# Kernel optimization log

Measured on AMD Instinct MI355X. Metric: run time of the kernel, lower is better.

## Reference

```python
import jax, jax.numpy as jnp
import numpy as np

B, T, D = 2, 2048, 1024
H, HD = 16, 64           # num_heads, head_dim (key_dim = value_dim = H*HD = D)
K = 4                    # short conv kernel size
EPS = 1e-6


def setup_inputs() -> dict:
    key = jax.random.key(0)
    ks = jax.random.split(key, 16)
    w = lambda k, shape, s=0.02: jax.random.normal(k, shape, jnp.float32) * s
    dt = jnp.exp(jax.random.uniform(ks[12], (H,)) * (np.log(0.1) - np.log(0.001)) + np.log(0.001))
    dt = jnp.clip(dt, 0.0001, None)
    return {
        "hidden_states": jax.random.normal(ks[0], (B, T, D), jnp.float32),
        "Wq": w(ks[1], (H * HD, D)),
        "Wk": w(ks[2], (H * HD, D)),
        "Wv": w(ks[3], (H * HD, D)),
        "Wa": w(ks[4], (H, D)),
        "Wb": w(ks[5], (H, D)),
        "Wg": w(ks[6], (H * HD, D)),
        "Wo": w(ks[7], (D, H * HD)),
        "q_norm_w": jnp.ones((HD,), jnp.float32),
        "k_norm_w": jnp.ones((HD,), jnp.float32),
        "o_norm_w": jnp.ones((HD,), jnp.float32),
        "A_log": jnp.log(jax.random.uniform(ks[11], (H,), jnp.float32, 0.5, 8.0)),
        "dt_bias": dt + jnp.log(-jnp.expm1(-dt)),
        "conv_q_w": w(ks[13], (H * HD, K), 0.2),
        "conv_k_w": w(ks[14], (H * HD, K), 0.2),
        "conv_v_w": w(ks[15], (H * HD, K), 0.2),
    }


def _short_conv_silu(x, w):
    # causal depthwise conv1d (kernel K) + SiLU; x: [B,T,C], w: [C,K]
    xc = jnp.transpose(x, (0, 2, 1))                       # [B,C,T]
    y = jax.lax.conv_general_dilated(
        xc, w[:, None, :], (1,), [(w.shape[-1] - 1, 0)],
        dimension_numbers=("NCH", "OIH", "NCH"), feature_group_count=w.shape[0])
    y = jnp.transpose(y, (0, 2, 1))
    return y * jax.nn.sigmoid(y)


def _rmsnorm(x, w):
    return x * jax.lax.rsqrt(jnp.mean(x * x, -1, keepdims=True) + EPS) * w


def _l2norm(x):
    return x * jax.lax.rsqrt(jnp.sum(x * x, -1, keepdims=True) + EPS)


def _forward(hidden_states, Wq, Wk, Wv, Wa, Wb, Wg, Wo,
             q_norm_w, k_norm_w, o_norm_w, A_log, dt_bias,
             conv_q_w, conv_k_w, conv_v_w):
    h = hidden_states
    q = _short_conv_silu(h @ Wq.T, conv_q_w).reshape(B, T, H, HD)
    k = _short_conv_silu(h @ Wk.T, conv_k_w).reshape(B, T, H, HD)
    v = _short_conv_silu(h @ Wv.T, conv_v_w).reshape(B, T, H, HD)
    q = _l2norm(_rmsnorm(q, q_norm_w))
    k = _l2norm(_rmsnorm(k, k_norm_w))
    beta = jax.nn.sigmoid(h @ Wb.T)                                  # [B,T,H]
    g = -jnp.exp(A_log) * jax.nn.softplus(h @ Wa.T + dt_bias)        # [B,T,H]
    scale = HD ** -0.5

    def step(S, inp):  # S: [B,H,dk,dv]
        qt, kt, vt, gt, bt = inp
        S = S * jnp.exp(gt)[:, :, None, None]
        kv = jnp.einsum("bhk,bhkv->bhv", kt, S)
        delta = (vt - kv) * bt[..., None]
        S = S + jnp.einsum("bhk,bhv->bhkv", kt, delta)
        o = jnp.einsum("bhk,bhkv->bhv", qt * scale, S)
        return S, o

    tm = lambda x: jnp.swapaxes(x, 0, 1)  # [B,T,...] -> [T,B,...]
    S0 = jnp.zeros((B, H, HD, HD), jnp.float32)
    _, o = jax.lax.scan(step, S0, (tm(q), tm(k), tm(v), tm(g), tm(beta)))
    o = jnp.swapaxes(o, 0, 1)                                        # [B,T,H,HD]

    gv = (h @ Wg.T).reshape(B, T, H, HD)
    o = _rmsnorm(o, o_norm_w) * (gv * jax.nn.sigmoid(gv))            # swish gate
    return o.reshape(B, T, H * HD) @ Wo.T


def reference(hidden_states, Wq, Wk, Wv, Wa, Wb, Wg, Wo,
              q_norm_w, k_norm_w, o_norm_w, A_log, dt_bias,
              conv_q_w, conv_k_w, conv_v_w):
    return _forward(hidden_states, Wq, Wk, Wv, Wa, Wb, Wg, Wo,
                    q_norm_w, k_norm_w, o_norm_w, A_log, dt_bias,
                    conv_q_w, conv_k_w, conv_v_w)
```

## Files before the change

kernel.cpp:

```cpp
#include <hip/hip_runtime.h>
#include <cstdint>
#include <cstddef>

#define B_ 2
#define T_ 2048
#define D_ 1024
#define H_ 16
#define HD_ 64
#define NC_ 32

typedef unsigned short u16;
typedef __attribute__((ext_vector_type(8))) short bf16x8;
typedef __attribute__((ext_vector_type(4))) float f32x4;

__device__ __forceinline__ float dot4(float4 a, float4 b, float acc) {
  return fmaf(a.x, b.x, fmaf(a.y, b.y, fmaf(a.z, b.z, fmaf(a.w, b.w, acc))));
}
__device__ __forceinline__ u16 f2bf(float f) {
  unsigned u = __float_as_uint(f);
  u += 0x7fffu + ((u >> 16) & 1u);
  return (u16)(u >> 16);
}
__device__ __forceinline__ float bf2f(u16 v) {
  return __uint_as_float(((unsigned)v) << 16);
}
__device__ __forceinline__ float4 ld4bf(const u16* p) {
  uint2 v = *(const uint2*)p;
  return float4{__uint_as_float(v.x << 16),
                __uint_as_float(v.x & 0xffff0000u),
                __uint_as_float(v.y << 16),
                __uint_as_float(v.y & 0xffff0000u)};
}
__device__ __forceinline__ bf16x8 pack8(float4 a, float4 b) {
  union { u16 us[8]; bf16x8 v; } p;
  p.us[0] = f2bf(a.x); p.us[1] = f2bf(a.y); p.us[2] = f2bf(a.z); p.us[3] = f2bf(a.w);
  p.us[4] = f2bf(b.x); p.us[5] = f2bf(b.y); p.us[6] = f2bf(b.z); p.us[7] = f2bf(b.w);
  return p.v;
}
__device__ __forceinline__ void glds16(const u16* g, u16* l) {
  __builtin_amdgcn_global_load_lds(
      (const __attribute__((address_space(1))) void*)g,
      (__attribute__((address_space(3))) void*)l, 16, 0, 0);
}
__device__ __forceinline__ float4 conv4(float4 x0, float4 x1, float4 x2, float4 x3,
                                        const float4* w) {
  float4 y;
  y.x = fmaf(w[0].x, x0.x, fmaf(w[0].y, x1.x, fmaf(w[0].z, x2.x, w[0].w * x3.x)));
  y.y = fmaf(w[1].x, x0.y, fmaf(w[1].y, x1.y, fmaf(w[1].z, x2.y, w[1].w * x3.y)));
  y.z = fmaf(w[2].x, x0.z, fmaf(w[2].y, x1.z, fmaf(w[2].z, x2.z, w[2].w * x3.z)));
  y.w = fmaf(w[3].x, x0.w, fmaf(w[3].y, x1.w, fmaf(w[3].z, x2.w, w[3].w * x3.w)));
  return y;
}
__device__ __forceinline__ float4 silu4(float4 a) {
  return float4{a.x / (1.f + __expf(-a.x)), a.y / (1.f + __expf(-a.y)),
                a.z / (1.f + __expf(-a.z)), a.w / (1.f + __expf(-a.w))};
}

__global__ __launch_bounds__(256) void cvt_all(
    const float* __restrict__ h, const float* __restrict__ w0,
    const float* __restrict__ w1, const float* __restrict__ w2,
    const float* __restrict__ w3, const float* __restrict__ w4,
    u16* __restrict__ h_bf, u16* __restrict__ wb)
{
  const int blk = blockIdx.x;
  const float* src;
  u16* dst;
  int lb;
  if (blk < 2048) { src = h; dst = h_bf; lb = blk; }
  else {
    int k = (blk - 2048) >> 9, r = (blk - 2048) & 511;
    src = k == 0 ? w0 : k == 1 ? w1 : k == 2 ? w2 : k == 3 ? w3 : w4;
    dst = wb + (size_t)k * 1048576;
    lb = r;
  }
  int i = (lb * 256 + threadIdx.x) * 8;
  float4 v0 = *(const float4*)(src + i);
  float4 v1 = *(const float4*)(src + i + 4);
  union { u16 us[8]; uint4 u4; } p;
  p.us[0] = f2bf(v0.x); p.us[1] = f2bf(v0.y); p.us[2] = f2bf(v0.z); p.us[3] = f2bf(v0.w);
  p.us[4] = f2bf(v1.x); p.us[5] = f2bf(v1.y); p.us[6] = f2bf(v1.z); p.us[7] = f2bf(v1.w);
  *(uint4*)(dst + i) = p.u4;
}

__device__ __forceinline__ void gemm_core256bf(const u16* __restrict__ A,
    const u16* __restrict__ Bw, u16* __restrict__ C,
    u16* As, u16* Bs, int row0, int col0, int K, int N)
{
  const int tid = threadIdx.x;
  const int lane = tid & 63, wave = tid >> 6;
  const int wr = (wave >> 1) * 128, wc = (wave & 1) * 64;
  const int lr = lane & 15, lkq = lane >> 4;
  const int lkp = (lkq ^ ((lr >> 1) & 3)) * 8;
  const int rql = (lane >> 2);
  const int cql = (((lane & 3) ^ ((rql >> 1) & 3))) * 8;
  const u16* gA[4];
  const u16* gB[2];
  #pragma unroll
  for (int i = 0; i < 4; ++i)
    gA[i] = A + (size_t)(row0 + (wave + 4*i) * 16 + rql) * K + cql;
  #pragma unroll
  for (int j = 0; j < 2; ++j)
    gB[j] = Bw + (size_t)(col0 + (wave + 4*j) * 16 + rql) * K + cql;

  f32x4 acc[8][4];
  #pragma unroll
  for (int i = 0; i < 8; ++i)
    #pragma unroll
    for (int j = 0; j < 4; ++j) acc[i][j] = f32x4{0.f, 0.f, 0.f, 0.f};

  auto STAGE = [&](int buf, int kt) {
    u16* ab = As + buf * 8192;
    u16* bb = Bs + buf * 4096;
    #pragma unroll
    for (int i = 0; i < 4; ++i) glds16(gA[i] + kt * 32, ab + (wave + 4*i) * 512);
    #pragma unroll
    for (int j = 0; j < 2; ++j) glds16(gB[j] + kt * 32, bb + (wave + 4*j) * 512);
  };

  const int KT = K >> 5;
  STAGE(0, 0);
  STAGE(1, 1);
  int cur = 0;
  for (int kt = 0; kt < KT; ++kt) {
    if (kt + 2 < KT) {
      STAGE(cur == 0 ? 2 : (cur == 1 ? 0 : 1), kt + 2);
      asm volatile("s_waitcnt vmcnt(12)" ::: "memory");
    } else if (kt + 1 < KT) {
      asm volatile("s_waitcnt vmcnt(6)" ::: "memory");
    } else {
      asm volatile("s_waitcnt vmcnt(0)" ::: "memory");
    }
    __builtin_amdgcn_s_barrier();
    __builtin_amdgcn_sched_barrier(0);
    const u16* Asc = As + cur * 8192;
    const u16* Bsc = Bs + cur * 4096;
    bf16x8 af[8], bf[4];
    #pragma unroll
    for (int i = 0; i < 8; ++i) af[i] = *(const bf16x8*)&Asc[(wr + i * 16 + lr) * 32 + lkp];
    #pragma unroll
    for (int j = 0; j < 4; ++j) bf[j] = *(const bf16x8*)&Bsc[(wc + j * 16 + lr) * 32 + lkp];
    #pragma unroll
    for (int i = 0; i < 8; ++i)
      #pragma unroll
      for (int j = 0; j < 4; ++j)
        acc[i][j] = __builtin_amdgcn_mfma_f32_16x16x32_bf16(af[i], bf[j], acc[i][j], 0, 0, 0);
    __builtin_amdgcn_sched_barrier(0);
    __builtin_amdgcn_s_barrier();
    cur = (cur == 2) ? 0 : cur + 1;
  }
  const int orow = row0 + wr + lkq * 4;
  const int ocol = col0 + wc + lr;
  #pragma unroll
  for (int i = 0; i < 8; ++i)
    #pragma unroll
    for (int j = 0; j < 4; ++j)
      #pragma unroll
      for (int r = 0; r < 4; ++r)
        C[(size_t)(orow + i * 16 + r) * N + ocol + j * 16] = f2bf(acc[i][j][r]);
}

__device__ __forceinline__ void gemm_core128(const u16* __restrict__ A,
    const u16* __restrict__ Bw, float* __restrict__ C,
    u16* As, u16* Bs, int row0, int col0, int K, int N)
{
  const int tid = threadIdx.x;
  const int lane = tid & 63, wave = tid >> 6;
  const int wr = (wave >> 1) * 64, wc = (wave & 1) * 64;
  const int lr = lane & 15;
  const int lkp = (((lane >> 4) ^ ((lr >> 1) & 3))) * 8;
  const int rql = (lane >> 2);
  const int cql = (((lane & 3) ^ ((rql >> 1) & 3))) * 8;
  const u16* gA0 = A + (size_t)(row0 + wave * 16 + rql) * K + cql;
  const u16* gA1 = A + (size_t)(row0 + (wave + 4) * 16 + rql) * K + cql;
  const u16* gB0 = Bw + (size_t)(col0 + wave * 16 + rql) * K + cql;
  const u16* gB1 = Bw + (size_t)(col0 + (wave + 4) * 16 + rql) * K + cql;

  f32x4 acc[4][4];
  #pragma unroll
  for (int i = 0; i < 4; ++i)
    #pragma unroll
    for (int j = 0; j < 4; ++j) acc[i][j] = f32x4{0.f, 0.f, 0.f, 0.f};

  auto STAGE = [&](int buf, int kt) {
    u16* ab = As + buf * 4096;
    u16* bb = Bs + buf * 4096;
    glds16(gA0 + kt * 32, ab + wave * 512);
    glds16(gA1 + kt * 32, ab + (wave + 4) * 512);
    glds16(gB0 + kt * 32, bb + wave * 512);
    glds16(gB1 + kt * 32, bb + (wave + 4) * 512);
  };

  const int KT = K >> 5;
  STAGE(0, 0);
  STAGE(1, 1);
  int cur = 0;
  for (int kt = 0; kt < KT; ++kt) {
    if (kt + 2 < KT) {
      STAGE(cur == 0 ? 2 : (cur == 1 ? 0 : 1), kt + 2);
      asm volatile("s_waitcnt vmcnt(8)" ::: "memory");
    } else if (kt + 1 < KT) {
      asm volatile("s_waitcnt vmcnt(4)" ::: "memory");
    } else {
      asm volatile("s_waitcnt vmcnt(0)" ::: "memory");
    }
    __builtin_amdgcn_s_barrier();
    __builtin_amdgcn_sched_barrier(0);
    const u16* Asc = As + cur * 4096;
    const u16* Bsc = Bs + cur * 4096;
    bf16x8 af[4], bf[4];
    #pragma unroll
    for (int i = 0; i < 4; ++i) af[i] = *(const bf16x8*)&Asc[(wr + i * 16 + lr) * 32 + lkp];
    #pragma unroll
    for (int j = 0; j < 4; ++j) bf[j] = *(const bf16x8*)&Bsc[(wc + j * 16 + lr) * 32 + lkp];
    #pragma unroll
    for (int i = 0; i < 4; ++i)
      #pragma unroll
      for (int j = 0; j < 4; ++j)
        acc[i][j] = __builtin_amdgcn_mfma_f32_16x16x32_bf16(af[i], bf[j], acc[i][j], 0, 0, 0);
    __builtin_amdgcn_sched_barrier(0);
    __builtin_amdgcn_s_barrier();
    cur = (cur == 2) ? 0 : cur + 1;
  }
  const int orow = row0 + wr + (lane >> 4) * 4;
  const int ocol = col0 + wc + lr;
  #pragma unroll
  for (int i = 0; i < 4; ++i)
    #pragma unroll
    for (int j = 0; j < 4; ++j)
      #pragma unroll
      for (int r = 0; r < 4; ++r)
        C[(size_t)(orow + i * 16 + r) * N + ocol + j * 16] = acc[i][j][r];
}

__global__ __launch_bounds__(256) void gemm_bf16_4(const u16* __restrict__ A,
    const u16* __restrict__ W0, const u16* __restrict__ W1,
    const u16* __restrict__ W2, const u16* __restrict__ W3,
    u16* __restrict__ C0, u16* __restrict__ C1,
    u16* __restrict__ C2, u16* __restrict__ C3)
{
  __shared__ u16 As[3 * 256 * 32];
  __shared__ u16 Bs[3 * 128 * 32];
  const int sel = blockIdx.y >> 3;
  const u16* Bw = sel == 0 ? W0 : sel == 1 ? W1 : sel == 2 ? W2 : W3;
  u16* C = sel == 0 ? C0 : sel == 1 ? C1 : sel == 2 ? C2 : C3;
  gemm_core256bf(A, Bw, C, As, Bs, blockIdx.x * 256, (blockIdx.y & 7) * 128, 1024, 1024);
}

__global__ __launch_bounds__(256) void gemm_bf16_1(const u16* __restrict__ A,
    const u16* __restrict__ Bw, float* __restrict__ C)
{
  __shared__ u16 As[3 * 128 * 32];
  __shared__ u16 Bs[3 * 128 * 32];
  gemm_core128(A, Bw, C, As, Bs, blockIdx.x * 128, blockIdx.y * 128, 1024, 1024);
}

#define SPW 261
__global__ __launch_bounds__(256) void smallproj(const float* __restrict__ Hs,
    const float* __restrict__ Wa, const float* __restrict__ Wb,
    const float* __restrict__ Alog, const float* __restrict__ dtb,
    float* __restrict__ Gout, float* __restrict__ Bout)
{
  __shared__ float hT[16][SPW];
  __shared__ float wT[32][SPW];
  const int row0 = blockIdx.x * 16;
  const int tid = threadIdx.x;
  const int r = tid >> 5;
  const int c = tid & 31;
  float a0 = 0.f, a1 = 0.f;
  for (int kc = 0; kc < 4; ++kc) {
    const int k0 = kc * 256;
    #pragma unroll
    for (int i = 0; i < 4; ++i) {
      int e4 = tid + i * 256;
      int rr = e4 >> 6, k4 = (e4 & 63) * 4;
      *(float4*)&hT[rr][k4] = *(const float4*)&Hs[(size_t)(row0 + rr) * D_ + k0 + k4];
    }
    #pragma unroll
    for (int i = 0; i < 8; ++i) {
      int e4 = tid + i * 256;
      int rr = e4 >> 6, k4 = (e4 & 63) * 4;
      const float* wsrc = (rr < 16) ? (Wa + (size_t)rr * D_) : (Wb + (size_t)(rr - 16) * D_);
      *(float4*)&wT[rr][k4] = *(const float4*)&wsrc[k0 + k4];
    }
    __syncthreads();
    #pragma unroll 8
    for (int k = 0; k < 256; k += 4) {
      float4 wv = *(const float4*)&wT[c][k];
      float4 h0 = *(const float4*)&hT[r][k];
      float4 h1 = *(const float4*)&hT[r + 8][k];
      a0 = dot4(h0, wv, a0);
      a1 = dot4(h1, wv, a1);
    }
    __syncthreads();
  }
  if (c < 16) {
    const float al = -__expf(Alog[c]);
    const float db = dtb[c];
    float x0 = a0 + db, x1 = a1 + db;
    float sp0 = fmaxf(x0, 0.f) + log1pf(__expf(-fabsf(x0)));
    float sp1 = fmaxf(x1, 0.f) + log1pf(__expf(-fabsf(x1)));
    Gout[(size_t)(row0 + r) * H_ + c] = al * sp0;
    Gout[(size_t)(row0 + r + 8) * H_ + c] = al * sp1;
  } else {
    const int hd = c - 16;
    Bout[(size_t)(row0 + r) * H_ + hd] = 1.f / (1.f + __expf(-a0));
    Bout[(size_t)(row0 + r + 8) * H_ + hd] = 1.f / (1.f + __expf(-a1));
  }
}

__global__ __launch_bounds__(256) void p1_chunk(
    const u16* __restrict__ Kp, const u16* __restrict__ Vp,
    const float* __restrict__ Gg, const float* __restrict__ Bb,
    const float* __restrict__ ckw, const float* __restrict__ cvw,
    const float* __restrict__ knw,
    u16* __restrict__ Ubf, u16* __restrict__ Wbf, u16* __restrict__ Kcb,
    float* __restrict__ Gcum, float* __restrict__ Mbuf, float* __restrict__ Nbuf)
{
  __shared__ u16 Kbf[64][72];
  __shared__ float Am[64][68];
  __shared__ float XT[128][68];
  __shared__ float gc[64], bet[64];
  const int bhc = blockIdx.x;
  const int bh = bhc >> 5, c = bhc & 31;
  const int b = bh >> 4, h = bh & 15;
  const int tid = threadIdx.x;
  const int lane = tid & 63, wave = tid >> 6;
  const int lr = lane & 15, lkq = lane >> 4;
  const size_t rowbase = ((size_t)b*T_ + c*64)*H_ + h;
  const int c4 = (tid & 15) * 4;
  const int hh64 = h * 64;

  if (tid < 64) {
    float gv = Gg[rowbase + (size_t)tid*H_];
    #pragma unroll
    for (int off = 1; off < 64; off <<= 1) {
      float up = __shfl_up(gv, off, 64);
      if (tid >= off) gv += up;
    }
    gc[tid] = gv;
    Gcum[(size_t)bhc*64 + tid] = gv;
    bet[tid] = Bb[rowbase + (size_t)tid*H_];
  }

  {
    float4 wk[4];
    float nwv[4];
    #pragma unroll
    for (int cc = 0; cc < 4; ++cc) {
      wk[cc] = *(const float4*)(ckw + (hh64 + c4 + cc) * 4);
      nwv[cc] = knw[c4 + cc];
    }
    #pragma unroll
    for (int k = 0; k < 4; ++k) {
      const int t = (tid >> 4) + k * 16;
      const int gt = c * 64 + t;
      const u16* src = Kp + (rowbase + (size_t)t * H_) * 64 + c4;
      float4 x3 = ld4bf(src);
      float4 x2 = (gt >= 1) ? ld4bf(src - D_)   : float4{0,0,0,0};
      float4 x1 = (gt >= 2) ? ld4bf(src - 2*D_) : float4{0,0,0,0};
      float4 x0 = (gt >= 3) ? ld4bf(src - 3*D_) : float4{0,0,0,0};
      float4 y = silu4(conv4(x0, x1, x2, x3, wk));
      float ss = fmaf(y.x, y.x, fmaf(y.y, y.y, fmaf(y.z, y.z, y.w * y.w)));
      ss += __shfl_xor(ss, 1); ss += __shfl_xor(ss, 2);
      ss += __shfl_xor(ss, 4); ss += __shfl_xor(ss, 8);
      const float inv1 = rsqrtf(ss * (1.f/64.f) + 1e-6f);
      float4 z = {y.x*inv1*nwv[0], y.y*inv1*nwv[1], y.z*inv1*nwv[2], y.w*inv1*nwv[3]};
      float s2 = fmaf(z.x, z.x, fmaf(z.y, z.y, fmaf(z.z, z.z, z.w * z.w)));
      s2 += __shfl_xor(s2, 1); s2 += __shfl_xor(s2, 2);
      s2 += __shfl_xor(s2, 4); s2 += __shfl_xor(s2, 8);
      const float inv2 = rsqrtf(s2 + 1e-6f);
      u16 tmp[4] = {f2bf(z.x*inv2), f2bf(z.y*inv2), f2bf(z.z*inv2), f2bf(z.w*inv2)};
      *(uint2*)&Kbf[t][c4] = *(uint2*)tmp;
      *(uint2*)&Kcb[(size_t)bhc*4096 + (size_t)t*64 + c4] = *(uint2*)tmp;
    }
  }
  __syncthreads();

  {
    bf16x8 afA[2];
    #pragma unroll
    for (int ks = 0; ks < 2; ++ks)
      afA[ks] = *(const bf16x8*)&Kbf[16*wave + lr][ks*32 + lkq*8];
    __builtin_amdgcn_s_setprio(1);
    #pragma unroll
    for (int j = 0; j < 4; ++j) {
      f32x4 accA = f32x4{0.f, 0.f, 0.f, 0.f};
      #pragma unroll
      for (int ks = 0; ks < 2; ++ks) {
        bf16x8 bfr = *(const bf16x8*)&Kbf[16*j + lr][ks*32 + lkq*8];
        accA = __builtin_amdgcn_mfma_f32_16x16x32_bf16(afA[ks], bfr, accA, 0, 0, 0);
      }
      const int s = 16*j + lr;
      #pragma unroll
      for (int r = 0; r < 4; ++r) {
        int t = 16*wave + lkq*4 + r;
        Am[t][s] = (s < t) ? bet[t] * __expf(gc[t] - gc[s]) * accA[r] : 0.f;
      }
    }
    __builtin_amdgcn_s_setprio(0);
  }
  {
    float4 wv[4];
    #pragma unroll
    for (int cc = 0; cc < 4; ++cc)
      wv[cc] = *(const float4*)(cvw + (hh64 + c4 + cc) * 4);
    #pragma unroll
    for (int k = 0; k < 4; ++k) {
      const int t = (tid >> 4) + k * 16;
      const int gt = c * 64 + t;
      const u16* src = Vp + (rowbase + (size_t)t * H_) * 64 + c4;
      float4 x3 = ld4bf(src);
      float4 x2 = (gt >= 1) ? ld4bf(src - D_)   : float4{0,0,0,0};
      float4 x1 = (gt >= 2) ? ld4bf(src - 2*D_) : float4{0,0,0,0};
      float4 x0 = (gt >= 3) ? ld4bf(src - 3*D_) : float4{0,0,0,0};
      float4 vv = silu4(conv4(x0, x1, x2, x3, wv));
      const float bt = bet[t];
      const float ek = bt * __expf(gc[t]);
      XT[c4+0][t] = bt * vv.x; XT[c4+1][t] = bt * vv.y;
      XT[c4+2][t] = bt * vv.z; XT[c4+3][t] = bt * vv.w;
      XT[64+c4+0][t] = ek * bf2f(Kbf[t][c4+0]);
      XT[64+c4+1][t] = ek * bf2f(Kbf[t][c4+1]);
      XT[64+c4+2][t] = ek * bf2f(Kbf[t][c4+2]);
      XT[64+c4+3][t] = ek * bf2f(Kbf[t][c4+3]);
    }
  }
  __syncthreads();

  for (int st = 0; st < 4; ++st) {
    if (st > 0) {
      const int nks = (st == 3) ? 2 : 1;
      f32x4 accU0 = f32x4{0.f,0.f,0.f,0.f}, accU1 = f32x4{0.f,0.f,0.f,0.f};
      __builtin_amdgcn_s_setprio(1);
      for (int ks = 0; ks < nks; ++ks) {
        const int m0 = ks*32 + lkq*8;
        bf16x8 af;
        if (m0 + 8 <= 16*st) {
          float4 a0 = *(const float4*)&Am[16*st + lr][m0];
          float4 a1 = *(const float4*)&Am[16*st + lr][m0 + 4];
          af = pack8(a0, a1);
        } else {
          af = bf16x8{0,0,0,0,0,0,0,0};
        }
        {
          const int cb = (wave*2 + 0) * 16;
          float4 b0 = *(const float4*)&XT[cb + lr][m0];
          float4 b1 = *(const float4*)&XT[cb + lr][m0 + 4];
          accU0 = __builtin_amdgcn_mfma_f32_16x16x32_bf16(af, pack8(b0, b1), accU0, 0, 0, 0);
        }
        {
          const int cb = (wave*2 + 1) * 16;
          float4 b0 = *(const float4*)&XT[cb + lr][m0];
          float4 b1 = *(const float4*)&XT[cb + lr][m0 + 4];
          accU1 = __builtin_amdgcn_mfma_f32_16x16x32_bf16(af, pack8(b0, b1), accU1, 0, 0, 0);
        }
      }
      __builtin_amdgcn_s_setprio(0);
      #pragma unroll
      for (int r = 0; r < 4; ++r) {
        const int t = 16*st + lkq*4 + r;
        XT[(wave*2+0)*16 + lr][t] -= accU0[r];
        XT[(wave*2+1)*16 + lr][t] -= accU1[r];
      }
      __syncthreads();
    }
    if (tid < 128) {
      const int bs = 16*st;
      float x[16];
      #pragma unroll
      for (int q = 0; q < 4; ++q)
        *(float4*)&x[q*4] = *(const float4*)&XT[tid][bs + q*4];
      #pragma unroll
      for (int tau = 1; tau < 16; ++tau) {
        float a = 0.f, a2 = 0.f;
        #pragma unroll
        for (int m = 0; m < tau; m += 2) {
          a = fmaf(Am[bs+tau][bs+m], x[m], a);
          if (m + 1 < tau) a2 = fmaf(Am[bs+tau][bs+m+1], x[m+1], a2);
        }
        x[tau] -= (a + a2);
      }
      #pragma unroll
      for (int q = 0; q < 4; ++q)
        *(float4*)&XT[tid][bs + q*4] = *(const float4*)&x[q*4];
    }
    __syncthreads();
  }

  for (int e = tid; e < 4096; e += 256) {
    int t = e >> 6, j = e & 63;
    Ubf[(size_t)bhc*4096 + e] = f2bf(XT[j][t]);
    Wbf[(size_t)bhc*4096 + e] = f2bf(XT[64+j][t]);
  }

  u16* KTb = (u16*)&Am[0][0];
  if (tid < 64) bet[tid] = __expf(gc[63] - gc[tid]);
  __syncthreads();
  for (int e4 = tid; e4 < 1024; e4 += 256) {
    int t = e4 >> 4, a4 = (e4 & 15) * 4;
    u16 k0 = Kbf[t][a4+0], k1 = Kbf[t][a4+1], k2 = Kbf[t][a4+2], k3 = Kbf[t][a4+3];
    KTb[(a4+0)*72 + t] = k0;
    KTb[(a4+1)*72 + t] = k1;
    KTb[(a4+2)*72 + t] = k2;
    KTb[(a4+3)*72 + t] = k3;
  }
  __syncthreads();

  bf16x8 afK[2];
  #pragma unroll
  for (int ks = 0; ks < 2; ++ks)
    afK[ks] = *(const bf16x8*)&KTb[(16*wave + lr)*72 + ks*32 + lkq*8];
  const float bC = __expf(gc[63]);
  const size_t ob = (size_t)bhc * 4096;
  #pragma unroll
  for (int j = 0; j < 4; ++j) {
    f32x4 aM = f32x4{0.f,0.f,0.f,0.f}, aN = f32x4{0.f,0.f,0.f,0.f};
    __builtin_amdgcn_s_setprio(1);
    #pragma unroll
    for (int ks = 0; ks < 2; ++ks) {
      const int m0 = ks*32 + lkq*8;
      float4 sc0 = *(const float4*)&bet[m0];
      float4 sc1 = *(const float4*)&bet[m0 + 4];
      float4 w0 = *(const float4*)&XT[64 + 16*j + lr][m0];
      float4 w1 = *(const float4*)&XT[64 + 16*j + lr][m0 + 4];
      float4 u0 = *(const float4*)&XT[16*j + lr][m0];
      float4 u1 = *(const float4*)&XT[16*j + lr][m0 + 4];
      w0.x*=sc0.x; w0.y*=sc0.y; w0.z*=sc0.z; w0.w*=sc0.w;
      w1.x*=sc1.x; w1.y*=sc1.y; w1.z*=sc1.z; w1.w*=sc1.w;
      u0.x*=sc0.x; u0.y*=sc0.y; u0.z*=sc0.z; u0.w*=sc0.w;
      u1.x*=sc1.x; u1.y*=sc1.y; u1.z*=sc1.z; u1.w*=sc1.w;
      aM = __builtin_amdgcn_mfma_f32_16x16x32_bf16(afK[ks], pack8(w0, w1), aM, 0, 0, 0);
      aN = __builtin_amdgcn_mfma_f32_16x16x32_bf16(afK[ks], pack8(u0, u1), aN, 0, 0, 0);
    }
    __builtin_amdgcn_s_setprio(0);
    const int cc = 16*j + lr;
    #pragma unroll
    for (int r = 0; r < 4; ++r) {
      const int a = 16*wave + lkq*4 + r;
      Mbuf[ob + (size_t)a*64 + cc] = (a == cc ? bC : 0.f) - aM[r];
      Nbuf[ob + (size_t)a*64 + cc] = aN[r];
    }
  }
}

__global__ __launch_bounds__(256) void pscanA(float* __restrict__ Mbuf,
    float* __restrict__ Nbuf)
{
  __shared__ float OM[2][64][68];
  __shared__ float ON[2][64][68];
  __shared__ float NM[2][64][68];
  const int blk = blockIdx.x;
  const int bh = blk >> 3, g = blk & 7;
  const size_t s0 = ((size_t)bh * 32 + g * 4) * 4096;
  const int tid = threadIdx.x;
  const int p0 = (tid >> 4) * 4;
  const int q0 = (tid & 15) * 4;
  for (int e4 = tid; e4 < 1024; e4 += 256) {
    int r = e4 >> 4, c4 = (e4 & 15) * 4;
    *(float4*)&OM[0][r][c4] = *(const float4*)&Mbuf[s0 + (size_t)r*64 + c4];
    *(float4*)&ON[0][r][c4] = *(const float4*)&Nbuf[s0 + (size_t)r*64 + c4];
    *(float4*)&NM[0][r][c4] = *(const float4*)&Mbuf[s0 + 4096 + (size_t)r*64 + c4];
  }
  __syncthreads();
  for (int s = 0; s < 3; ++s) {
    const int cur = s & 1, nxt = cur ^ 1;
    const size_t wslot = s0 + (size_t)(s + 1) * 4096;
    if (s < 2) {
      for (int e4 = tid; e4 < 1024; e4 += 256) {
        int r = e4 >> 4, c4 = (e4 & 15) * 4;
        *(float4*)&NM[nxt][r][c4] = *(const float4*)&Mbuf[wslot + 4096 + (size_t)r*64 + c4];
      }
    }
    float aM[4][4], aN[4][4];
    #pragma unroll
    for (int r = 0; r < 4; ++r) {
      float4 nv = *(const float4*)&Nbuf[wslot + (size_t)(p0+r)*64 + q0];
      aM[r][0]=0.f; aM[r][1]=0.f; aM[r][2]=0.f; aM[r][3]=0.f;
      aN[r][0]=nv.x; aN[r][1]=nv.y; aN[r][2]=nv.z; aN[r][3]=nv.w;
    }
    for (int m4 = 0; m4 < 64; m4 += 4) {
      float xv[4][4];
      #pragma unroll
      for (int r = 0; r < 4; ++r) {
        float4 v = *(const float4*)&NM[cur][p0+r][m4];
        xv[r][0]=v.x; xv[r][1]=v.y; xv[r][2]=v.z; xv[r][3]=v.w;
      }
      #pragma unroll
      for (int mm = 0; mm < 4; ++mm) {
        float4 ym = *(const float4*)&OM[cur][m4+mm][q0];
        float4 yn = *(const float4*)&ON[cur][m4+mm][q0];
        #pragma unroll
        for (int r = 0; r < 4; ++r) {
          aM[r][0] = fmaf(xv[r][mm], ym.x, aM[r][0]);
          aM[r][1] = fmaf(xv[r][mm], ym.y, aM[r][1]);
          aM[r][2] = fmaf(xv[r][mm], ym.z, aM[r][2]);
          aM[r][3] = fmaf(xv[r][mm], ym.w, aM[r][3]);
          aN[r][0] = fmaf(xv[r][mm], yn.x, aN[r][0]);
          aN[r][1] = fmaf(xv[r][mm], yn.y, aN[r][1]);
          aN[r][2] = fmaf(xv[r][mm], yn.z, aN[r][2]);
          aN[r][3] = fmaf(xv[r][mm], yn.w, aN[r][3]);
        }
      }
    }
    #pragma unroll
    for (int r = 0; r < 4; ++r) {
      float4 vm = {aM[r][0], aM[r][1], aM[r][2], aM[r][3]};
      float4 vn = {aN[r][0], aN[r][1], aN[r][2], aN[r][3]};
      *(float4*)&Mbuf[wslot + (size_t)(p0+r)*64 + q0] = vm;
      *(float4*)&Nbuf[wslot + (size_t)(p0+r)*64 + q0] = vn;
      *(float4*)&OM[nxt][p0+r][q0] = vm;
      *(float4*)&ON[nxt][p0+r][q0] = vn;
    }
    __syncthreads();
  }
}

__global__ __launch_bounds__(256) void pscanB(const float* __restrict__ Mbuf,
    const float* __restrict__ Nbuf, float* __restrict__ S0b)
{
  __shared__ float ST[2][64][68];
  __shared__ float MT[64][68];
  const int bh = blockIdx.x;
  const size_t base = (size_t)bh * 32 * 4096;
  const int tid = threadIdx.x;
  const int j0 = (tid >> 4) * 4, a0 = tid & 15;
  for (int e4 = tid; e4 < 1024; e4 += 256) {
    int r = e4 >> 4, c4 = (e4 & 15) * 4;
    *(float4*)&ST[0][r][c4] = float4{0.f, 0.f, 0.f, 0.f};
    *(float4*)&S0b[base + (size_t)r*64 + c4] = float4{0.f, 0.f, 0.f, 0.f};
  }
  for (int g = 0; g < 7; ++g) {
    const int cur = g & 1, nxt = cur ^ 1;
    const size_t tslot = base + (size_t)(4*g + 3) * 4096;
    for (int e4 = tid; e4 < 1024; e4 += 256) {
      int r = e4 >> 4, c4 = (e4 & 15) * 4;
      *(float4*)&MT[r][c4] = *(const float4*)&Mbuf[tslot + (size_t)r*64 + c4];
    }
    float acc[4][4];
    #pragma unroll
    for (int r = 0; r < 4; ++r)
      #pragma unroll
      for (int s = 0; s < 4; ++s)
        acc[r][s] = Nbuf[tslot + (size_t)(a0 + 16*s)*64 + j0 + r];
    __syncthreads();
    for (int k4 = 0; k4 < 64; k4 += 4) {
      float4 xr[4];
      #pragma unroll
      for (int r = 0; r < 4; ++r) xr[r] = *(const float4*)&ST[cur][j0+r][k4];
      #pragma unroll
      for (int s = 0; s < 4; ++s) {
        float4 yv = *(const float4*)&MT[a0 + 16*s][k4];
        #pragma unroll
        for (int r = 0; r < 4; ++r) acc[r][s] = dot4(xr[r], yv, acc[r][s]);
      }
    }
    const size_t oslot = base + (size_t)(4*(g+1)) * 4096;
    #pragma unroll
    for (int r = 0; r < 4; ++r)
      #pragma unroll
      for (int s = 0; s < 4; ++s) {
        ST[nxt][j0+r][a0 + 16*s] = acc[r][s];
        S0b[oslot + (size_t)(j0+r)*64 + a0 + 16*s] = acc[r][s];
      }
    __syncthreads();
  }
}

__global__ __launch_bounds__(256) void p3_out(
    const u16* __restrict__ Qp, const u16* __restrict__ Kcb,
    const float* __restrict__ cqw, const float* __restrict__ qnw,
    const float* __restrict__ Gcum, const float* __restrict__ S0b,
    const float* __restrict__ Mbuf, const float* __restrict__ Nbuf,
    const u16* __restrict__ Ubf, const u16* __restrict__ Wbfg,
    const u16* __restrict__ GV, const float* __restrict__ onw,
    u16* __restrict__ OG)
{
  __shared__ u16 Qbf[64][72];
  __shared__ u16 Kbf[64][72];
  __shared__ u16 S0T[64][72];
  __shared__ u16 Wbf[64][72];
  __shared__ u16 Pbf[64][72];
  __shared__ u16 DsT[64][72];
  __shared__ float gcs[64];
  __shared__ float onws[64];
  const int bhc = blockIdx.x;
  const int bh = bhc >> 5, c = bhc & 31;
  const int b = bh >> 4, h = bh & 15;
  const int tid = threadIdx.x;
  const int lane = tid & 63, wave = tid >> 6;
  const int lr = lane & 15, lkq = lane >> 4;
  const size_t rowbase = ((size_t)b*T_ + c*64)*H_ + h;
  const int c4 = (tid & 15) * 4;
  const int hh64 = h * 64;
  const int ii = c & 3;
  if (tid < 64) { gcs[tid] = Gcum[(size_t)bhc*64 + tid]; onws[tid] = onw[tid]; }

  {
    float4 wq[4];
    float nwv[4];
    #pragma unroll
    for (int cc = 0; cc < 4; ++cc) {
      wq[cc] = *(const float4*)(cqw + (hh64 + c4 + cc) * 4);
      nwv[cc] = qnw[c4 + cc];
    }
    #pragma unroll
    for (int k = 0; k < 4; ++k) {
      const int t = (tid >> 4) + k * 16;
      const int gt = c * 64 + t;
      const u16* src = Qp + (rowbase + (size_t)t * H_) * 64 + c4;
      float4 x3 = ld4bf(src);
      float4 x2 = (gt >= 1) ? ld4bf(src - D_)   : float4{0,0,0,0};
      float4 x1 = (gt >= 2) ? ld4bf(src - 2*D_) : float4{0,0,0,0};
      float4 x0 = (gt >= 3) ? ld4bf(src - 3*D_) : float4{0,0,0,0};
      float4 y = silu4(conv4(x0, x1, x2, x3, wq));
      float ss = fmaf(y.x, y.x, fmaf(y.y, y.y, fmaf(y.z, y.z, y.w * y.w)));
      ss += __shfl_xor(ss, 1); ss += __shfl_xor(ss, 2);
      ss += __shfl_xor(ss, 4); ss += __shfl_xor(ss, 8);
      const float inv1 = rsqrtf(ss * (1.f/64.f) + 1e-6f);
      float4 z = {y.x*inv1*nwv[0], y.y*inv1*nwv[1], y.z*inv1*nwv[2], y.w*inv1*nwv[3]};
      float s2 = fmaf(z.x, z.x, fmaf(z.y, z.y, fmaf(z.z, z.z, z.w * z.w)));
      s2 += __shfl_xor(s2, 1); s2 += __shfl_xor(s2, 2);
      s2 += __shfl_xor(s2, 4); s2 += __shfl_xor(s2, 8);
      const float inv2 = rsqrtf(s2 + 1e-6f) * 0.125f;
      u16 tmp[4] = {f2bf(z.x*inv2), f2bf(z.y*inv2), f2bf(z.z*inv2), f2bf(z.w*inv2)};
      *(uint2*)&Qbf[t][c4] = *(uint2*)tmp;
    }
  }
  for (int e4 = tid; e4 < 1024; e4 += 256) {
    int t = e4 >> 4, d4 = (e4 & 15) * 4;
    *(uint2*)&Kbf[t][d4] = *(const uint2*)&Kcb[(size_t)bhc*4096 + (size_t)t*64 + d4];
    *(uint2*)&Wbf[t][d4] = *(const uint2*)&Wbfg[(size_t)bhc*4096 + (size_t)t*64 + d4];
  }
  if (ii == 0) {
    for (int e4 = tid; e4 < 1024; e4 += 256) {
      int t = e4 >> 4, d4 = (e4 & 15) * 4;
      float4 sv = *(const float4*)&S0b[(size_t)bhc*4096 + (size_t)t*64 + d4];
      u16 as[4] = {f2bf(sv.x), f2bf(sv.y), f2bf(sv.z), f2bf(sv.w)};
      *(uint2*)&S0T[t][d4] = *(uint2*)as;
    }
  } else {
    const size_t gslot = ((size_t)bh*NC_ + (c & ~3)) * 4096;
    const size_t pslot = ((size_t)bh*NC_ + c - 1) * 4096;
    for (int e4 = tid; e4 < 1024; e4 += 256) {
      int t = e4 >> 4, d4 = (e4 & 15) * 4;
      float4 sg = *(const float4*)&S0b[gslot + (size_t)t*64 + d4];
      float4 mp = *(const float4*)&Mbuf[pslot + (size_t)t*64 + d4];
      u16 a1[4] = {f2bf(sg.x), f2bf(sg.y), f2bf(sg.z), f2bf(sg.w)};
      u16 a2[4] = {f2bf(mp.x), f2bf(mp.y), f2bf(mp.z), f2bf(mp.w)};
      *(uint2*)&DsT[t][d4] = *(uint2*)a1;
      *(uint2*)&Pbf[t][d4] = *(uint2*)a2;
    }
  }
  __syncthreads();

  if (ii != 0) {
    const size_t pslot = ((size_t)bh*NC_ + c - 1) * 4096;
    bf16x8 ag[2];
    #pragma unroll
    for (int ks = 0; ks < 2; ++ks)
      ag[ks] = *(const bf16x8*)&DsT[16*wave + lr][ks*32 + lkq*8];
    #pragma unroll
    for (int ab = 0; ab < 4; ++ab) {
      f32x4 cin;
      {
        float4 nv = *(const float4*)&Nbuf[pslot + (size_t)(16*ab + lr)*64 + 16*wave + lkq*4];
        cin[0] = nv.x; cin[1] = nv.y; cin[2] = nv.z; cin[3] = nv.w;
      }
      __builtin_amdgcn_s_setprio(1);
      #pragma unroll
      for (int ks = 0; ks < 2; ++ks) {
        bf16x8 bm = *(const bf16x8*)&Pbf[16*ab + lr][ks*32 + lkq*8];
        cin = __builtin_amdgcn_mfma_f32_16x16x32_bf16(ag[ks], bm, cin, 0, 0, 0);
      }
      __builtin_amdgcn_s_setprio(0);
      #pragma unroll
      for (int r = 0; r < 4; ++r)
        S0T[16*wave + lkq*4 + r][16*ab + lr] = f2bf(cin[r]);
    }
    __syncthreads();
  }

  const int trow0 = 16*wave + lkq*4;
  bf16x8 aq[2], aw[2];
  #pragma unroll
  for (int ks = 0; ks < 2; ++ks) {
    aq[ks] = *(const bf16x8*)&Qbf[16*wave + lr][ks*32 + lkq*8];
    aw[ks] = *(const bf16x8*)&Wbf[16*wave + lr][ks*32 + lkq*8];
  }
  float gct[4], egt[4];
  #pragma unroll
  for (int r = 0; r < 4; ++r) { gct[r] = gcs[trow0 + r]; egt[r] = __expf(gct[r]); }

  #pragma unroll
  for (int j = 0; j < 4; ++j) {
    f32x4 pa = f32x4{0.f,0.f,0.f,0.f};
    __builtin_amdgcn_s_setprio(1);
    #pragma unroll
    for (int ks = 0; ks < 2; ++ks) {
      bf16x8 bk = *(const bf16x8*)&Kbf[16*j + lr][ks*32 + lkq*8];
      pa = __builtin_amdgcn_mfma_f32_16x16x32_bf16(aq[ks], bk, pa, 0, 0, 0);
    }
    __builtin_amdgcn_s_setprio(0);
    const int s = 16*j + lr;
    const float gs = gcs[s];
    #pragma unroll
    for (int r = 0; r < 4; ++r) {
      const int t = trow0 + r;
      float val = (s <= t) ? __expf(gct[r] - gs) * pa[r] : 0.f;
      Pbf[t][s] = f2bf(val);
    }
  }

  #pragma unroll
  for (int j = 0; j < 4; ++j) {
    f32x4 da = f32x4{0.f,0.f,0.f,0.f};
    __builtin_amdgcn_s_setprio(1);
    #pragma unroll
    for (int ks = 0; ks < 2; ++ks) {
      bf16x8 bs = *(const bf16x8*)&S0T[16*j + lr][ks*32 + lkq*8];
      da = __builtin_amdgcn_mfma_f32_16x16x32_bf16(aw[ks], bs, da, 0, 0, 0);
    }
    __builtin_amdgcn_s_setprio(0);
    const int jj = 16*j + lr;
    #pragma unroll
    for (int r = 0; r < 4; ++r) {
      const int s = trow0 + r;
      float dv = bf2f(Ubf[(size_t)bhc*4096 + (size_t)s*64 + jj]) - da[r];
      DsT[jj][s] = f2bf(dv);
    }
  }

  f32x4 oacc[4];
  #pragma unroll
  for (int j = 0; j < 4; ++j) {
    f32x4 oa = f32x4{0.f,0.f,0.f,0.f};
    __builtin_amdgcn_s_setprio(1);
    #pragma unroll
    for (int ks = 0; ks < 2; ++ks) {
      bf16x8 bs = *(const bf16x8*)&S0T[16*j + lr][ks*32 + lkq*8];
      oa = __builtin_amdgcn_mfma_f32_16x16x32_bf16(aq[ks], bs, oa, 0, 0, 0);
    }
    __builtin_amdgcn_s_setprio(0);
    #pragma unroll
    for (int r = 0; r < 4; ++r) oa[r] *= egt[r];
    oacc[j] = oa;
  }
  __syncthreads();

  bf16x8 ap[2];
  #pragma unroll
  for (int ks = 0; ks < 2; ++ks)
    ap[ks] = *(const bf16x8*)&Pbf[16*wave + lr][ks*32 + lkq*8];
  __builtin_amdgcn_s_setprio(1);
  #pragma unroll
  for (int j = 0; j < 4; ++j) {
    #pragma unroll
    for (int ks = 0; ks < 2; ++ks) {
      bf16x8 bd = *(const bf16x8*)&DsT[16*j + lr][ks*32 + lkq*8];
      oacc[j] = __builtin_amdgcn_mfma_f32_16x16x32_bf16(ap[ks], bd, oacc[j], 0, 0, 0);
    }
  }
  __builtin_amdgcn_s_setprio(0);

  #pragma unroll
  for (int r = 0; r < 4; ++r) {
    float ss = 0.f;
    #pragma unroll
    for (int jq = 0; jq < 4; ++jq) ss = fmaf(oacc[jq][r], oacc[jq][r], ss);
    ss += __shfl_xor(ss, 1); ss += __shfl_xor(ss, 2);
    ss += __shfl_xor(ss, 4); ss += __shfl_xor(ss, 8);
    const float inv = rsqrtf(ss * (1.f/64.f) + 1e-6f);
    const int t = trow0 + r;
    const size_t rowoff = ((size_t)b*T_ + (size_t)c*64 + t) * D_ + h*64;
    #pragma unroll
    for (int jq = 0; jq < 4; ++jq) {
      const int jj = 16*jq + lr;
      float y = oacc[jq][r] * inv * onws[jj];
      float gv = bf2f(GV[rowoff + jj]);
      OG[rowoff + jj] = f2bf(y * gv / (1.f + __expf(-gv)));
    }
  }
}

extern "C" void kernel_launch(void* const* d_in, const int* in_sizes, int n_in,
                              void* d_out, int out_size, void* d_ws, size_t ws_size,
                              hipStream_t stream) {
  const float* h    = (const float*)d_in[0];
  const float* Wq   = (const float*)d_in[1];
  const float* Wk   = (const float*)d_in[2];
  const float* Wv   = (const float*)d_in[3];
  const float* Wa   = (const float*)d_in[4];
  const float* Wb   = (const float*)d_in[5];
  const float* Wg   = (const float*)d_in[6];
  const float* Wo   = (const float*)d_in[7];
  const float* qnw  = (const float*)d_in[8];
  const float* knw  = (const float*)d_in[9];
  const float* onw  = (const float*)d_in[10];
  const float* Alog = (const float*)d_in[11];
  const float* dtb  = (const float*)d_in[12];
  const float* cqw  = (const float*)d_in[13];
  const float* ckw  = (const float*)d_in[14];
  const float* cvw  = (const float*)d_in[15];
  float* out = (float*)d_out;
  float* ws  = (float*)d_ws;

  const size_t NB = (size_t)B_ * T_ * D_;
  float* qp   = ws;
  float* kp   = ws + 1*NB;
  float* vp   = ws + 2*NB;
  float* gvp  = ws + 3*NB;
  float* qc   = ws + 4*NB;
  float* kc   = ws + 5*NB;
  float* vc   = ws + 6*NB;
  float* mb   = ws + 7*NB;
  float* wbf  = ws + 8*NB;
  float* gb   = ws + 8*NB + 5*524288;
  float* bb   = gb + (size_t)B_*T_*H_;
  float* Gc   = bb + (size_t)B_*T_*H_;

  u16* h_bf  = (u16*)mb;
  u16* og_bf = (u16*)kp;
  u16* w_bf  = (u16*)wbf;
  u16* wq_bf = w_bf + 0*1048576;
  u16* wk_bf = w_bf + 1*1048576;
  u16* wv_bf = w_bf + 2*1048576;
  u16* wg_bf = w_bf + 3*1048576;
  u16* wo_bf = w_bf + 4*1048576;

  u16*   Qpb  = (u16*)qp;
  u16*   Kpb  = (u16*)kp;
  u16*   Vpb  = (u16*)vp;
  u16*   GVb  = (u16*)gvp;
  u16*   Ubf  = (u16*)qc;
  u16*   Wbfp = (u16*)qc + NB;
  u16*   Kcb  = (u16*)kc;
  float* Nbuf = vc;
  float* S0b  = vp;
  float* Mbuf = mb;

  cvt_all<<<4608, 256, 0, stream>>>(h, Wq, Wk, Wv, Wg, Wo, h_bf, w_bf);

  gemm_bf16_4<<<dim3(16, 32), 256, 0, stream>>>(h_bf, wq_bf, wk_bf, wv_bf, wg_bf,
                                                 Qpb, Kpb, Vpb, GVb);
  smallproj<<<256, 256, 0, stream>>>(h, Wa, Wb, Alog, dtb, gb, bb);

  p1_chunk<<<B_*H_*NC_, 256, 0, stream>>>(Kpb, Vpb, gb, bb, ckw, cvw, knw,
                                          Ubf, Wbfp, Kcb, Gc, Mbuf, Nbuf);
  pscanA<<<B_*H_*8, 256, 0, stream>>>(Mbuf, Nbuf);
  pscanB<<<B_*H_, 256, 0, stream>>>(Mbuf, Nbuf, S0b);
  p3_out<<<B_*H_*NC_, 256, 0, stream>>>(Qpb, Kcb, cqw, qnw, Gc, S0b, Mbuf, Nbuf,
                                        Ubf, Wbfp, GVb, onw, og_bf);

  gemm_bf16_1<<<dim3(32, 8), 256, 0, stream>>>(og_bf, wo_bf, out);
}
```

Before: 217.9 us.

## Restructure fused QKVG GEMM to 256x256 tiles with 8 waves and split-MFMA prefetch

The four-way projection GEMM moves from 256x128 tiles with 4 waves to 256x256 tiles with 8 waves in one block per CU. The grid shrinks from 512 to 256 blocks. The loop prefetches three stages ahead, issues the next global-to-LDS load between two halves of the MFMA work, and raises wave priority around the MFMA bursts. The intent is more data reuse per loaded tile and better overlap of memory with compute. In exchange, 256 blocks on a chip with many CUs may give a poor tail, and the larger LDS use limits occupancy.

```diff
diff --git a/kernel.cpp b/kernel.cpp
--- a/kernel.cpp
+++ b/kernel.cpp
@@ -82,25 +82,25 @@
   *(uint4*)(dst + i) = p.u4;
 }
 
-__device__ __forceinline__ void gemm_core256bf(const u16* __restrict__ A,
-    const u16* __restrict__ Bw, u16* __restrict__ C,
-    u16* As, u16* Bs, int row0, int col0, int K, int N)
+__global__ __launch_bounds__(512, 1) void gemm_bf16_4(const u16* __restrict__ A,
+    const u16* __restrict__ W0, const u16* __restrict__ W1,
+    const u16* __restrict__ W2, const u16* __restrict__ W3,
+    u16* __restrict__ C0, u16* __restrict__ C1,
+    u16* __restrict__ C2, u16* __restrict__ C3)
 {
+  __shared__ u16 As[3 * 256 * 32];
+  __shared__ u16 Bs[3 * 256 * 32];
+  const int K = 1024, N = 1024;
+  const int sel = blockIdx.y >> 2;
+  const u16* Bw = sel == 0 ? W0 : sel == 1 ? W1 : sel == 2 ? W2 : W3;
+  u16* C = sel == 0 ? C0 : sel == 1 ? C1 : sel == 2 ? C2 : C3;
+  const int row0 = blockIdx.x * 256;
+  const int col0 = (blockIdx.y & 3) * 256;
   const int tid = threadIdx.x;
   const int lane = tid & 63, wave = tid >> 6;
-  const int wr = (wave >> 1) * 128, wc = (wave & 1) * 64;
+  const int wm = wave >> 2, wn = wave & 3;
   const int lr = lane & 15, lkq = lane >> 4;
   const int lkp = (lkq ^ ((lr >> 1) & 3)) * 8;
-  const int rql = (lane >> 2);
-  const int cql = (((lane & 3) ^ ((rql >> 1) & 3))) * 8;
-  const u16* gA[4];
-  const u16* gB[2];
-  #pragma unroll
-  for (int i = 0; i < 4; ++i)
-    gA[i] = A + (size_t)(row0 + (wave + 4*i) * 16 + rql) * K + cql;
-  #pragma unroll
-  for (int j = 0; j < 2; ++j)
-    gB[j] = Bw + (size_t)(col0 + (wave + 4*j) * 16 + rql) * K + cql;
 
   f32x4 acc[8][4];
   #pragma unroll
@@ -110,46 +110,65 @@
 
   auto STAGE = [&](int buf, int kt) {
     u16* ab = As + buf * 8192;
-    u16* bb = Bs + buf * 4096;
-    #pragma unroll
-    for (int i = 0; i < 4; ++i) glds16(gA[i] + kt * 32, ab + (wave + 4*i) * 512);
-    #pragma unroll
-    for (int j = 0; j < 2; ++j) glds16(gB[j] + kt * 32, bb + (wave + 4*j) * 512);
+    u16* bb = Bs + buf * 8192;
+    #pragma unroll
+    for (int g = 0; g < 2; ++g) {
+      const int idx = g * 512 + tid;
+      const int rr = idx >> 2, cl = idx & 3;
+      const int csw = (cl ^ ((rr >> 1) & 3)) * 8;
+      glds16(A  + (size_t)(row0 + rr) * K + kt * 32 + csw, ab + idx * 8);
+      glds16(Bw + (size_t)(col0 + rr) * K + kt * 32 + csw, bb + idx * 8);
+    }
   };
 
   const int KT = K >> 5;
-  STAGE(0, 0);
-  STAGE(1, 1);
-  int cur = 0;
+  STAGE(0, 0); STAGE(1, 1); STAGE(2, 2);
+  asm volatile("s_waitcnt vmcnt(8)" ::: "memory");
+  __builtin_amdgcn_s_barrier();
+  __builtin_amdgcn_sched_barrier(0);
+
   for (int kt = 0; kt < KT; ++kt) {
-    if (kt + 2 < KT) {
-      STAGE(cur == 0 ? 2 : (cur == 1 ? 0 : 1), kt + 2);
-      asm volatile("s_waitcnt vmcnt(12)" ::: "memory");
-    } else if (kt + 1 < KT) {
-      asm volatile("s_waitcnt vmcnt(6)" ::: "memory");
+    const int cur = kt % 3;
+    const u16* Asc = As + cur * 8192;
+    const u16* Bsc = Bs + cur * 8192;
+    bf16x8 af[8], bfr[4];
+    #pragma unroll
+    for (int i = 0; i < 8; ++i)
+      af[i] = *(const bf16x8*)&Asc[(wm * 128 + i * 16 + lr) * 32 + lkp];
+    #pragma unroll
+    for (int j = 0; j < 4; ++j)
+      bfr[j] = *(const bf16x8*)&Bsc[(wn * 64 + j * 16 + lr) * 32 + lkp];
+    __builtin_amdgcn_s_setprio(1);
+    #pragma unroll
+    for (int i = 0; i < 4; ++i)
+      #pragma unroll
+      for (int j = 0; j < 4; ++j)
+        acc[i][j] = __builtin_amdgcn_mfma_f32_16x16x32_bf16(af[i], bfr[j], acc[i][j], 0, 0, 0);
+    __builtin_amdgcn_s_setprio(0);
+    asm volatile("s_waitcnt lgkmcnt(0)" ::: "memory");
+    __builtin_amdgcn_sched_barrier(0);
+    __builtin_amdgcn_s_barrier();
+    __builtin_amdgcn_sched_barrier(0);
+    if (kt + 3 < KT) {
+      STAGE(cur, kt + 3);
+      asm volatile("s_waitcnt vmcnt(4)" ::: "memory");
     } else {
       asm volatile("s_waitcnt vmcnt(0)" ::: "memory");
     }
+    __builtin_amdgcn_s_setprio(1);
+    #pragma unroll
+    for (int i = 4; i < 8; ++i)
+      #pragma unroll
+      for (int j = 0; j < 4; ++j)
+        acc[i][j] = __builtin_amdgcn_mfma_f32_16x16x32_bf16(af[i], bfr[j], acc[i][j], 0, 0, 0);
+    __builtin_amdgcn_s_setprio(0);
+    __builtin_amdgcn_sched_barrier(0);
     __builtin_amdgcn_s_barrier();
     __builtin_amdgcn_sched_barrier(0);
-    const u16* Asc = As + cur * 8192;
-    const u16* Bsc = Bs + cur * 4096;
-    bf16x8 af[8], bf[4];
-    #pragma unroll
-    for (int i = 0; i < 8; ++i) af[i] = *(const bf16x8*)&Asc[(wr + i * 16 + lr) * 32 + lkp];
-    #pragma unroll
-    for (int j = 0; j < 4; ++j) bf[j] = *(const bf16x8*)&Bsc[(wc + j * 16 + lr) * 32 + lkp];
-    #pragma unroll
-    for (int i = 0; i < 8; ++i)
-      #pragma unroll
-      for (int j = 0; j < 4; ++j)
-        acc[i][j] = __builtin_amdgcn_mfma_f32_16x16x32_bf16(af[i], bf[j], acc[i][j], 0, 0, 0);
-    __builtin_amdgcn_sched_barrier(0);
-    __builtin_amdgcn_s_barrier();
-    cur = (cur == 2) ? 0 : cur + 1;
-  }
-  const int orow = row0 + wr + lkq * 4;
-  const int ocol = col0 + wc + lr;
+  }
+
+  const int orow = row0 + wm * 128 + (lane >> 4) * 4;
+  const int ocol = col0 + wn * 64 + lr;
   #pragma unroll
   for (int i = 0; i < 8; ++i)
     #pragma unroll
@@ -230,20 +249,6 @@
       #pragma unroll
       for (int r = 0; r < 4; ++r)
         C[(size_t)(orow + i * 16 + r) * N + ocol + j * 16] = acc[i][j][r];
-}
-
-__global__ __launch_bounds__(256) void gemm_bf16_4(const u16* __restrict__ A,
-    const u16* __restrict__ W0, const u16* __restrict__ W1,
-    const u16* __restrict__ W2, const u16* __restrict__ W3,
-    u16* __restrict__ C0, u16* __restrict__ C1,
-    u16* __restrict__ C2, u16* __restrict__ C3)
-{
-  __shared__ u16 As[3 * 256 * 32];
-  __shared__ u16 Bs[3 * 128 * 32];
-  const int sel = blockIdx.y >> 3;
-  const u16* Bw = sel == 0 ? W0 : sel == 1 ? W1 : sel == 2 ? W2 : W3;
-  u16* C = sel == 0 ? C0 : sel == 1 ? C1 : sel == 2 ? C2 : C3;
-  gemm_core256bf(A, Bw, C, As, Bs, blockIdx.x * 256, (blockIdx.y & 7) * 128, 1024, 1024);
 }
 
 __global__ __launch_bounds__(256) void gemm_bf16_1(const u16* __restrict__ A,
@@ -939,7 +944,7 @@
 
   cvt_all<<<4608, 256, 0, stream>>>(h, Wq, Wk, Wv, Wg, Wo, h_bf, w_bf);
 
-  gemm_bf16_4<<<dim3(16, 32), 256, 0, stream>>>(h_bf, wq_bf, wk_bf, wv_bf, wg_bf,
+  gemm_bf16_4<<<dim3(16, 16), 512, 0, stream>>>(h_bf, wq_bf, wk_bf, wv_bf, wg_bf,
                                                  Qpb, Kpb, Vpb, GVb);
   smallproj<<<256, 256, 0, stream>>>(h, Wa, Wb, Alog, dtb, gb, bb);
 
```

Result: no change. 215.5 us (-1.1%).
